# Optimization experiments

Hardware: AMD Instinct MI355X
Metric: run time of the kernel (lower is better)

Reference implementation:

```python
import jax, jax.numpy as jnp
import numpy as np

B, D = 16384, 1024
H1, H2 = 512, 256
T = 3          # num_tasks
E_SH = 2       # num_shared_experts
E_SP = 2       # num_specific_experts
G = E_SH + E_SP


def setup_inputs() -> dict:
    key = jax.random.key(0)
    ks = jax.random.split(key, 8)
    def glorot(k, shape, fan_in, fan_out):
        return jax.random.normal(k, shape, jnp.float32) * jnp.sqrt(2.0 / (fan_in + fan_out))
    return {
        "x": jax.random.normal(ks[0], (B, D), jnp.float32),
        "shared_W1": glorot(ks[1], (E_SH, D, H1), D, H1),
        "shared_b1": jnp.zeros((E_SH, H1), jnp.float32),
        "shared_W2": glorot(ks[2], (E_SH, H1, H2), H1, H2),
        "shared_b2": jnp.zeros((E_SH, H2), jnp.float32),
        "spec_W1": glorot(ks[3], (T, E_SP, D, H1), D, H1),
        "spec_b1": jnp.zeros((T, E_SP, H1), jnp.float32),
        "spec_W2": glorot(ks[4], (T, E_SP, H1, H2), H1, H2),
        "spec_b2": jnp.zeros((T, E_SP, H2), jnp.float32),
        "gate_W": glorot(ks[5], (T, D, G), D, G),
        "gate_b": jnp.zeros((T, G), jnp.float32),
    }


def reference(x, shared_W1, shared_b1, shared_W2, shared_b2,
              spec_W1, spec_b1, spec_W2, spec_b2, gate_W, gate_b):
    # Shared experts: two-layer MLP with relu, batched over experts. [B, E_SH, H2]
    sh = jax.nn.relu(jnp.einsum('bi,eih->beh', x, shared_W1) + shared_b1)
    sh = jax.nn.relu(jnp.einsum('beh,eho->beo', sh, shared_W2) + shared_b2)
    # Task-specific experts, batched over (task, expert). [B, T, E_SP, H2]
    sp = jax.nn.relu(jnp.einsum('bi,teih->bteh', x, spec_W1) + spec_b1)
    sp = jax.nn.relu(jnp.einsum('bteh,teho->bteo', sp, spec_W2) + spec_b2)
    # Gates: single linear layer per task + softmax over G=E_SH+E_SP experts. [B, T, G]
    gate = jax.nn.softmax(jnp.einsum('bi,tig->btg', x, gate_W) + gate_b, axis=-1)
    # Experts stacked in order: shared first, then specific (matches tf.stack order).
    sh_b = jnp.broadcast_to(sh[:, None], (B, T, E_SH, H2))
    experts = jnp.concatenate([sh_b, sp], axis=2)  # [B, T, G, H2]
    # Gate-weighted sum over the expert axis -> per-task outputs [B, T, H2]
    out = jnp.einsum('btgh,btg->bth', experts, gate)
    return out
```

## Files before the change

### kernel.cpp

```cpp
#include <hip/hip_runtime.h>
#include <hip/hip_bf16.h>
#include <stdint.h>

#define B_SZ 16384
#define D_SZ 1024
#define H1_SZ 512
#define H2_SZ 256
#define T_SZ 3
#define ESH 2
#define NE 8

typedef __bf16 bf16x8 __attribute__((ext_vector_type(8)));
typedef float f32x4 __attribute__((ext_vector_type(4)));
typedef unsigned short u16;
typedef u16 u16x8 __attribute__((ext_vector_type(8)));

__device__ __forceinline__ u16 f2bf(float f) {
  union { float f; uint32_t u; } v; v.f = f;
  uint32_t u = v.u;
  uint32_t r = (u + 0x7FFFu + ((u >> 16) & 1u)) >> 16;
  return (u16)r;
}
__device__ __forceinline__ float bf2f(u16 b) {
  union { uint32_t u; float f; } v; v.u = ((uint32_t)b) << 16;
  return v.f;
}

__device__ __forceinline__ void gload16(const u16* src, u16* dst_lds) {
  __builtin_amdgcn_global_load_lds(
      (const __attribute__((address_space(1))) void*)src,
      (__attribute__((address_space(3))) void*)dst_lds, 16, 0, 0);
}

__global__ __launch_bounds__(256) void cast_f32_to_bf16(
    const float* __restrict__ in, u16* __restrict__ out, int n8) {
  int i = blockIdx.x * blockDim.x + threadIdx.x;
  if (i >= n8) return;
  const float4* p = (const float4*)in + (size_t)i * 2;
  float4 a = p[0], b = p[1];
  u16x8 o;
  o[0] = f2bf(a.x); o[1] = f2bf(a.y); o[2] = f2bf(a.z); o[3] = f2bf(a.w);
  o[4] = f2bf(b.x); o[5] = f2bf(b.y); o[6] = f2bf(b.z); o[7] = f2bf(b.w);
  *((u16x8*)out + i) = o;
}

__global__ __launch_bounds__(256) void transpose_cast(
    const float* __restrict__ src, u16* __restrict__ dst, int K, int N) {
  __shared__ float tile[32][33];
  size_t e = blockIdx.z;
  const float* s = src + e * (size_t)K * N;
  u16* d = dst + e * (size_t)K * N;
  int n0 = blockIdx.x * 32, k0 = blockIdx.y * 32;
  int tx = threadIdx.x, ty = threadIdx.y;
#pragma unroll
  for (int i = ty; i < 32; i += 8)
    tile[i][tx] = s[(size_t)(k0 + i) * N + n0 + tx];
  __syncthreads();
#pragma unroll
  for (int i = ty; i < 32; i += 8)
    d[(size_t)(n0 + i) * K + k0 + tx] = f2bf(tile[tx][i]);
}

__global__ __launch_bounds__(512, 2) void gemm_ring(
    const u16* __restrict__ A, size_t strideAe,
    const u16* __restrict__ Bt,
    const float* __restrict__ bias_sh, const float* __restrict__ bias_sp,
    u16* __restrict__ C, int M, int N, int K, int ntn) {
  __shared__ __align__(16) u16 lds[4 * 16384];
  const int tid = threadIdx.x;
  const int wid = tid >> 6, lane = tid & 63;
  const int fr = lane & 15, fq = lane >> 4;
  const int wr = wid >> 2, wc = wid & 3;

  const int nwg = gridDim.x;
  const int bid = blockIdx.x;
  const int l = (bid & 7) * (nwg >> 3) + (bid >> 3);
  const int e = l & 7;
  const int rest = l >> 3;
  const int ntile = rest % ntn;
  const int mtile = rest / ntn;
  const int m0 = mtile * 256, n0 = ntile * 256;

  const u16* Ae = A + (size_t)e * strideAe;
  const u16* Be = Bt + (size_t)e * (size_t)N * K;
  const int NT = K >> 5;

  const int c0 = tid, c1 = 512 + tid;
  const int ar0 = c0 >> 2, as0 = (c0 & 3) ^ ((ar0 >> 1) & 3);
  const int ar1 = c1 >> 2, as1 = (c1 & 3) ^ ((ar1 >> 1) & 3);
  const u16* pA0 = Ae + (size_t)(m0 + ar0) * K + as0 * 8;
  const u16* pA1 = Ae + (size_t)(m0 + ar1) * K + as1 * 8;
  const u16* pB0 = Be + (size_t)(n0 + ar0) * K + as0 * 8;
  const u16* pB1 = Be + (size_t)(n0 + ar1) * K + as1 * 8;
  const int dst0 = (wid * 64) * 8;
  const int dst1 = (512 + wid * 64) * 8;

  int offA[8], offB[4];
#pragma unroll
  for (int m = 0; m < 8; ++m) {
    int r = wr * 128 + m * 16 + fr;
    offA[m] = r * 32 + ((fq ^ ((r >> 1) & 3)) * 8);
  }
#pragma unroll
  for (int n = 0; n < 4; ++n) {
    int cg = wc * 64 + n * 16 + fr;
    offB[n] = 8192 + cg * 32 + ((fq ^ ((cg >> 1) & 3)) * 8);
  }

  f32x4 acc[8][4] = {};

#define STAGE(t) do { const int sbs = ((t) & 3) * 16384;              \
    gload16(pA0 + (t) * 32, &lds[sbs + dst0]);                        \
    gload16(pA1 + (t) * 32, &lds[sbs + dst1]);                        \
    gload16(pB0 + (t) * 32, &lds[sbs + 8192 + dst0]);                 \
    gload16(pB1 + (t) * 32, &lds[sbs + 8192 + dst1]); } while (0)

  STAGE(0); STAGE(1); STAGE(2);
  asm volatile("s_waitcnt vmcnt(8)");
  __builtin_amdgcn_s_barrier();
  __builtin_amdgcn_sched_barrier(0);

  for (int t = 0; t < NT; ++t) {
    const u16* sl = &lds[(t & 3) * 16384];
    bf16x8 av[8], bv[4];
#pragma unroll
    for (int m = 0; m < 8; ++m) av[m] = *(const bf16x8*)&sl[offA[m]];
#pragma unroll
    for (int n = 0; n < 4; ++n) bv[n] = *(const bf16x8*)&sl[offB[n]];
    if (t + 3 < NT) STAGE(t + 3);
    __builtin_amdgcn_s_setprio(1);
#pragma unroll
    for (int m = 0; m < 8; ++m)
#pragma unroll
      for (int n = 0; n < 4; ++n)
        acc[m][n] = __builtin_amdgcn_mfma_f32_16x16x32_bf16(av[m], bv[n], acc[m][n], 0, 0, 0);
    __builtin_amdgcn_s_setprio(0);
    asm volatile("s_waitcnt vmcnt(8)");
    __builtin_amdgcn_s_barrier();
    __builtin_amdgcn_sched_barrier(0);
  }
#undef STAGE

  const float* bias = (e < ESH) ? (bias_sh + (size_t)e * N)
                                : (bias_sp + (size_t)(e - ESH) * N);
  u16* Ce = C + (size_t)e * (size_t)M * N;
  float bb[4];
#pragma unroll
  for (int n = 0; n < 4; ++n) bb[n] = bias[n0 + wc * 64 + n * 16 + fr];

  const int src = (tid >> 5);
  const int cc = (tid & 31) * 8;
#pragma unroll
  for (int half = 0; half < 2; ++half) {
    if (wr == half) {
#pragma unroll
      for (int m = 0; m < 8; ++m) {
#pragma unroll
        for (int n = 0; n < 4; ++n) {
          const int col = wc * 64 + n * 16 + fr;
          f32x4 a = acc[m][n];
#pragma unroll
          for (int r = 0; r < 4; ++r) {
            float v = a[r] + bb[n];
            v = v > 0.f ? v : 0.f;
            lds[(m * 16 + fq * 4 + r) * 256 + col] = f2bf(v);
          }
        }
      }
    }
    __builtin_amdgcn_s_barrier();
#pragma unroll
    for (int pass = 0; pass < 8; ++pass) {
      const int lr = pass * 16 + src;
      const int gr = m0 + half * 128 + lr;
      u16x8 vv = *(const u16x8*)&lds[lr * 256 + cc];
      *(u16x8*)&Ce[(size_t)gr * N + n0 + cc] = vv;
    }
    __builtin_amdgcn_s_barrier();
  }
}

__global__ __launch_bounds__(256) void gates_kernel(
    const float* __restrict__ x, const float* __restrict__ gW,
    const float* __restrict__ gb, float* __restrict__ gates) {
  __shared__ float gw[12][1024];
  const int tid = threadIdx.x;
  for (int i = tid; i < 12 * 1024; i += 256) {
    int tg = i >> 10, k = i & 1023;
    gw[tg][k] = gW[(size_t)(tg >> 2) * 4096 + (size_t)k * 4 + (tg & 3)];
  }
  __syncthreads();
  const int wid = tid >> 6, lane = tid & 63;
  const size_t b = (size_t)blockIdx.x * 4 + wid;
  const float* xr = x + b * 1024;
  float acc[12] = {};
  for (int kk = 0; kk < 16; ++kk) {
    float xv = xr[kk * 64 + lane];
#pragma unroll
    for (int t = 0; t < 12; ++t) acc[t] += xv * gw[t][kk * 64 + lane];
  }
#pragma unroll
  for (int off = 32; off >= 1; off >>= 1)
#pragma unroll
    for (int t = 0; t < 12; ++t) acc[t] += __shfl_xor(acc[t], off);
  if (lane == 0) {
    float* gr = gates + b * 12;
#pragma unroll
    for (int t = 0; t < 3; ++t) {
      float l0 = acc[t * 4 + 0] + gb[t * 4 + 0];
      float l1 = acc[t * 4 + 1] + gb[t * 4 + 1];
      float l2 = acc[t * 4 + 2] + gb[t * 4 + 2];
      float l3 = acc[t * 4 + 3] + gb[t * 4 + 3];
      float mx = fmaxf(fmaxf(l0, l1), fmaxf(l2, l3));
      float e0 = __expf(l0 - mx), e1 = __expf(l1 - mx);
      float e2 = __expf(l2 - mx), e3 = __expf(l3 - mx);
      float inv = 1.f / (e0 + e1 + e2 + e3);
      gr[t * 4 + 0] = e0 * inv; gr[t * 4 + 1] = e1 * inv;
      gr[t * 4 + 2] = e2 * inv; gr[t * 4 + 3] = e3 * inv;
    }
  }
}

__global__ __launch_bounds__(256) void combine_kernel(
    const u16* __restrict__ y2, const float* __restrict__ gates,
    float* __restrict__ out) {
  const int tid = threadIdx.x;
  const int rb = tid >> 5;
  const int hc = (tid & 31) * 8;
  const size_t b = (size_t)blockIdx.x * 8 + rb;
  const float* g = gates + b * 12;
  float acc0[8] = {}, acc1[8] = {}, acc2[8] = {};
#pragma unroll
  for (int e = 0; e < 8; ++e) {
    u16x8 v = *(const u16x8*)&y2[(size_t)e * B_SZ * H2_SZ + b * H2_SZ + hc];
    float f[8];
#pragma unroll
    for (int i = 0; i < 8; ++i) f[i] = bf2f(v[i]);
    if (e < 2) {
      float g0 = g[0 * 4 + e], g1 = g[1 * 4 + e], g2 = g[2 * 4 + e];
#pragma unroll
      for (int i = 0; i < 8; ++i) {
        acc0[i] += g0 * f[i]; acc1[i] += g1 * f[i]; acc2[i] += g2 * f[i];
      }
    } else {
      const int t = (e - 2) >> 1, gi = 2 + ((e - 2) & 1);
      float gv = g[t * 4 + gi];
      float* acc = (t == 0) ? acc0 : (t == 1) ? acc1 : acc2;
#pragma unroll
      for (int i = 0; i < 8; ++i) acc[i] += gv * f[i];
    }
  }
  float* o = out + b * (3 * 256);
  *(float4*)&o[0 * 256 + hc]     = make_float4(acc0[0], acc0[1], acc0[2], acc0[3]);
  *(float4*)&o[0 * 256 + hc + 4] = make_float4(acc0[4], acc0[5], acc0[6], acc0[7]);
  *(float4*)&o[1 * 256 + hc]     = make_float4(acc1[0], acc1[1], acc1[2], acc1[3]);
  *(float4*)&o[1 * 256 + hc + 4] = make_float4(acc1[4], acc1[5], acc1[6], acc1[7]);
  *(float4*)&o[2 * 256 + hc]     = make_float4(acc2[0], acc2[1], acc2[2], acc2[3]);
  *(float4*)&o[2 * 256 + hc + 4] = make_float4(acc2[4], acc2[5], acc2[6], acc2[7]);
}

extern "C" void kernel_launch(void* const* d_in, const int* in_sizes, int n_in,
                              void* d_out, int out_size, void* d_ws, size_t ws_size,
                              hipStream_t stream) {
  (void)in_sizes; (void)n_in; (void)out_size; (void)ws_size;
  const float* x   = (const float*)d_in[0];
  const float* sW1 = (const float*)d_in[1];
  const float* sb1 = (const float*)d_in[2];
  const float* sW2 = (const float*)d_in[3];
  const float* sb2 = (const float*)d_in[4];
  const float* pW1 = (const float*)d_in[5];
  const float* pb1 = (const float*)d_in[6];
  const float* pW2 = (const float*)d_in[7];
  const float* pb2 = (const float*)d_in[8];
  const float* gW  = (const float*)d_in[9];
  const float* gb  = (const float*)d_in[10];

  uint8_t* ws = (uint8_t*)d_ws;
  u16* xb    = (u16*)(ws);
  u16* w1t   = (u16*)(ws + 33554432);
  u16* w2t   = (u16*)(ws + 41943040);
  u16* y1    = (u16*)(ws + 44040192);
  u16* y2    = (u16*)(ws + 178257920);
  float* gts = (float*)(ws + 245366784);

  cast_f32_to_bf16<<<(B_SZ * D_SZ / 8 + 255) / 256, 256, 0, stream>>>(
      x, xb, B_SZ * D_SZ / 8);

  transpose_cast<<<dim3(512 / 32, 1024 / 32, 2), dim3(32, 8), 0, stream>>>(
      sW1, w1t, 1024, 512);
  transpose_cast<<<dim3(512 / 32, 1024 / 32, 6), dim3(32, 8), 0, stream>>>(
      pW1, w1t + (size_t)2 * 1024 * 512, 1024, 512);
  transpose_cast<<<dim3(256 / 32, 512 / 32, 2), dim3(32, 8), 0, stream>>>(
      sW2, w2t, 512, 256);
  transpose_cast<<<dim3(256 / 32, 512 / 32, 6), dim3(32, 8), 0, stream>>>(
      pW2, w2t + (size_t)2 * 512 * 256, 512, 256);

  gates_kernel<<<B_SZ / 4, 256, 0, stream>>>(x, gW, gb, gts);

  gemm_ring<<<(B_SZ / 256) * (512 / 256) * NE, 512, 0, stream>>>(
      xb, 0, w1t, sb1, pb1, y1, B_SZ, 512, 1024, 512 / 256);

  gemm_ring<<<(B_SZ / 256) * (256 / 256) * NE, 512, 0, stream>>>(
      y1, (size_t)B_SZ * 512, w2t, sb2, pb2, y2, B_SZ, 256, 512, 256 / 256);

  combine_kernel<<<B_SZ / 8, 256, 0, stream>>>(y2, gts, (float*)d_out);
}
```

Before: 324.1 us.

## Fuse preprocessing kernels and split GEMM K-loop into two-phase pipelined halves

Merges the four weight transpose-cast launches into one kernel and folds the x-to-bf16 cast into the gates kernel, so x is read once and fewer launches are issued. The GEMM is replaced by a two-phase variant. Each K-step splits the A loads and MFMAs into halves with interleaved barriers, and prefetch depth drops from 3 to 2 stages. The block-to-tile mapping no longer uses the XCD-aware remap, and the epilogue LDS row stride is padded to 264 to reduce bank conflicts. The extra barriers and shallower prefetch may expose memory latency, and dropping the remap may hurt L2 locality.

```diff
diff --git a/kernel.cpp b/kernel.cpp
--- a/kernel.cpp
+++ b/kernel.cpp
@@ -32,24 +32,26 @@
       (__attribute__((address_space(3))) void*)dst_lds, 16, 0, 0);
 }
 
-__global__ __launch_bounds__(256) void cast_f32_to_bf16(
-    const float* __restrict__ in, u16* __restrict__ out, int n8) {
-  int i = blockIdx.x * blockDim.x + threadIdx.x;
-  if (i >= n8) return;
-  const float4* p = (const float4*)in + (size_t)i * 2;
-  float4 a = p[0], b = p[1];
-  u16x8 o;
-  o[0] = f2bf(a.x); o[1] = f2bf(a.y); o[2] = f2bf(a.z); o[3] = f2bf(a.w);
-  o[4] = f2bf(b.x); o[5] = f2bf(b.y); o[6] = f2bf(b.z); o[7] = f2bf(b.w);
-  *((u16x8*)out + i) = o;
-}
-
-__global__ __launch_bounds__(256) void transpose_cast(
-    const float* __restrict__ src, u16* __restrict__ dst, int K, int N) {
+__global__ __launch_bounds__(256) void transpose_cast_all(
+    const float* __restrict__ sW1, const float* __restrict__ pW1,
+    const float* __restrict__ sW2, const float* __restrict__ pW2,
+    u16* __restrict__ w1t, u16* __restrict__ w2t) {
   __shared__ float tile[32][33];
-  size_t e = blockIdx.z;
-  const float* s = src + e * (size_t)K * N;
-  u16* d = dst + e * (size_t)K * N;
+  const int z = blockIdx.z;
+  int K, N;
+  const float* s;
+  u16* d;
+  if (z < 8) {
+    K = 1024; N = 512;
+    s = (z < 2) ? (sW1 + (size_t)z * K * N) : (pW1 + (size_t)(z - 2) * K * N);
+    d = w1t + (size_t)z * K * N;
+  } else {
+    K = 512; N = 256;
+    const int e = z - 8;
+    if (blockIdx.x >= 8 || blockIdx.y >= 16) return;
+    s = (e < 2) ? (sW2 + (size_t)e * K * N) : (pW2 + (size_t)(e - 2) * K * N);
+    d = w2t + (size_t)e * K * N;
+  }
   int n0 = blockIdx.x * 32, k0 = blockIdx.y * 32;
   int tx = threadIdx.x, ty = threadIdx.y;
 #pragma unroll
@@ -61,128 +63,10 @@
     d[(size_t)(n0 + i) * K + k0 + tx] = f2bf(tile[tx][i]);
 }
 
-__global__ __launch_bounds__(512, 2) void gemm_ring(
-    const u16* __restrict__ A, size_t strideAe,
-    const u16* __restrict__ Bt,
-    const float* __restrict__ bias_sh, const float* __restrict__ bias_sp,
-    u16* __restrict__ C, int M, int N, int K, int ntn) {
-  __shared__ __align__(16) u16 lds[4 * 16384];
-  const int tid = threadIdx.x;
-  const int wid = tid >> 6, lane = tid & 63;
-  const int fr = lane & 15, fq = lane >> 4;
-  const int wr = wid >> 2, wc = wid & 3;
-
-  const int nwg = gridDim.x;
-  const int bid = blockIdx.x;
-  const int l = (bid & 7) * (nwg >> 3) + (bid >> 3);
-  const int e = l & 7;
-  const int rest = l >> 3;
-  const int ntile = rest % ntn;
-  const int mtile = rest / ntn;
-  const int m0 = mtile * 256, n0 = ntile * 256;
-
-  const u16* Ae = A + (size_t)e * strideAe;
-  const u16* Be = Bt + (size_t)e * (size_t)N * K;
-  const int NT = K >> 5;
-
-  const int c0 = tid, c1 = 512 + tid;
-  const int ar0 = c0 >> 2, as0 = (c0 & 3) ^ ((ar0 >> 1) & 3);
-  const int ar1 = c1 >> 2, as1 = (c1 & 3) ^ ((ar1 >> 1) & 3);
-  const u16* pA0 = Ae + (size_t)(m0 + ar0) * K + as0 * 8;
-  const u16* pA1 = Ae + (size_t)(m0 + ar1) * K + as1 * 8;
-  const u16* pB0 = Be + (size_t)(n0 + ar0) * K + as0 * 8;
-  const u16* pB1 = Be + (size_t)(n0 + ar1) * K + as1 * 8;
-  const int dst0 = (wid * 64) * 8;
-  const int dst1 = (512 + wid * 64) * 8;
-
-  int offA[8], offB[4];
-#pragma unroll
-  for (int m = 0; m < 8; ++m) {
-    int r = wr * 128 + m * 16 + fr;
-    offA[m] = r * 32 + ((fq ^ ((r >> 1) & 3)) * 8);
-  }
-#pragma unroll
-  for (int n = 0; n < 4; ++n) {
-    int cg = wc * 64 + n * 16 + fr;
-    offB[n] = 8192 + cg * 32 + ((fq ^ ((cg >> 1) & 3)) * 8);
-  }
-
-  f32x4 acc[8][4] = {};
-
-#define STAGE(t) do { const int sbs = ((t) & 3) * 16384;              \
-    gload16(pA0 + (t) * 32, &lds[sbs + dst0]);                        \
-    gload16(pA1 + (t) * 32, &lds[sbs + dst1]);                        \
-    gload16(pB0 + (t) * 32, &lds[sbs + 8192 + dst0]);                 \
-    gload16(pB1 + (t) * 32, &lds[sbs + 8192 + dst1]); } while (0)
-
-  STAGE(0); STAGE(1); STAGE(2);
-  asm volatile("s_waitcnt vmcnt(8)");
-  __builtin_amdgcn_s_barrier();
-  __builtin_amdgcn_sched_barrier(0);
-
-  for (int t = 0; t < NT; ++t) {
-    const u16* sl = &lds[(t & 3) * 16384];
-    bf16x8 av[8], bv[4];
-#pragma unroll
-    for (int m = 0; m < 8; ++m) av[m] = *(const bf16x8*)&sl[offA[m]];
-#pragma unroll
-    for (int n = 0; n < 4; ++n) bv[n] = *(const bf16x8*)&sl[offB[n]];
-    if (t + 3 < NT) STAGE(t + 3);
-    __builtin_amdgcn_s_setprio(1);
-#pragma unroll
-    for (int m = 0; m < 8; ++m)
-#pragma unroll
-      for (int n = 0; n < 4; ++n)
-        acc[m][n] = __builtin_amdgcn_mfma_f32_16x16x32_bf16(av[m], bv[n], acc[m][n], 0, 0, 0);
-    __builtin_amdgcn_s_setprio(0);
-    asm volatile("s_waitcnt vmcnt(8)");
-    __builtin_amdgcn_s_barrier();
-    __builtin_amdgcn_sched_barrier(0);
-  }
-#undef STAGE
-
-  const float* bias = (e < ESH) ? (bias_sh + (size_t)e * N)
-                                : (bias_sp + (size_t)(e - ESH) * N);
-  u16* Ce = C + (size_t)e * (size_t)M * N;
-  float bb[4];
-#pragma unroll
-  for (int n = 0; n < 4; ++n) bb[n] = bias[n0 + wc * 64 + n * 16 + fr];
-
-  const int src = (tid >> 5);
-  const int cc = (tid & 31) * 8;
-#pragma unroll
-  for (int half = 0; half < 2; ++half) {
-    if (wr == half) {
-#pragma unroll
-      for (int m = 0; m < 8; ++m) {
-#pragma unroll
-        for (int n = 0; n < 4; ++n) {
-          const int col = wc * 64 + n * 16 + fr;
-          f32x4 a = acc[m][n];
-#pragma unroll
-          for (int r = 0; r < 4; ++r) {
-            float v = a[r] + bb[n];
-            v = v > 0.f ? v : 0.f;
-            lds[(m * 16 + fq * 4 + r) * 256 + col] = f2bf(v);
-          }
-        }
-      }
-    }
-    __builtin_amdgcn_s_barrier();
-#pragma unroll
-    for (int pass = 0; pass < 8; ++pass) {
-      const int lr = pass * 16 + src;
-      const int gr = m0 + half * 128 + lr;
-      u16x8 vv = *(const u16x8*)&lds[lr * 256 + cc];
-      *(u16x8*)&Ce[(size_t)gr * N + n0 + cc] = vv;
-    }
-    __builtin_amdgcn_s_barrier();
-  }
-}
-
-__global__ __launch_bounds__(256) void gates_kernel(
+__global__ __launch_bounds__(256) void gates_cast_kernel(
     const float* __restrict__ x, const float* __restrict__ gW,
-    const float* __restrict__ gb, float* __restrict__ gates) {
+    const float* __restrict__ gb, float* __restrict__ gates,
+    u16* __restrict__ xb) {
   __shared__ float gw[12][1024];
   const int tid = threadIdx.x;
   for (int i = tid; i < 12 * 1024; i += 256) {
@@ -193,9 +77,11 @@
   const int wid = tid >> 6, lane = tid & 63;
   const size_t b = (size_t)blockIdx.x * 4 + wid;
   const float* xr = x + b * 1024;
+  u16* xbr = xb + b * 1024;
   float acc[12] = {};
   for (int kk = 0; kk < 16; ++kk) {
     float xv = xr[kk * 64 + lane];
+    xbr[kk * 64 + lane] = f2bf(xv);
 #pragma unroll
     for (int t = 0; t < 12; ++t) acc[t] += xv * gw[t][kk * 64 + lane];
   }
@@ -218,6 +104,145 @@
       gr[t * 4 + 0] = e0 * inv; gr[t * 4 + 1] = e1 * inv;
       gr[t * 4 + 2] = e2 * inv; gr[t * 4 + 3] = e3 * inv;
     }
+  }
+}
+
+__global__ __launch_bounds__(512, 2) void gemm_2ph(
+    const u16* __restrict__ A, size_t strideAe,
+    const u16* __restrict__ Bt,
+    const float* __restrict__ bias_sh, const float* __restrict__ bias_sp,
+    u16* __restrict__ C, int M, int N, int K, int ntn_sh) {
+  __shared__ __align__(16) u16 lds[4 * 16384];
+  const int tid = threadIdx.x;
+  const int wid = tid >> 6, lane = tid & 63;
+  const int fr = lane & 15, fq = lane >> 4;
+  const int wr = wid >> 2, wc = wid & 3;
+
+  const int bid = blockIdx.x;
+  const int e = bid & 7;
+  const int rest = bid >> 3;
+  const int mtile = rest >> ntn_sh;
+  const int ntile = rest & ((1 << ntn_sh) - 1);
+  const int m0 = mtile * 256, n0 = ntile * 256;
+
+  const u16* Ae = A + (size_t)e * strideAe;
+  const u16* Be = Bt + (size_t)e * (size_t)N * K;
+  const int NT = K >> 5;
+
+  const int srow = tid >> 2;
+  const int sslot = (tid & 3) ^ ((tid >> 3) & 3);
+  const u16* pA[2];
+  const u16* pB[2];
+#pragma unroll
+  for (int h = 0; h < 2; ++h) {
+    pA[h] = Ae + (size_t)(m0 + h * 128 + srow) * K + sslot * 8;
+    pB[h] = Be + (size_t)(n0 + h * 128 + srow) * K + sslot * 8;
+  }
+  const int wdst = wid * 512;
+
+  int offA[8], offB[4];
+#pragma unroll
+  for (int m = 0; m < 8; ++m) {
+    int rr = wr * 128 + m * 16 + fr;
+    offA[m] = rr * 32 + ((fq ^ ((fr >> 1) & 3)) * 8);
+  }
+#pragma unroll
+  for (int n = 0; n < 4; ++n) {
+    int cg = wc * 64 + n * 16 + fr;
+    offB[n] = 8192 + cg * 32 + ((fq ^ ((fr >> 1) & 3)) * 8);
+  }
+
+  f32x4 acc[8][4] = {};
+
+#define STG_A(t) do { const int sbs = ((t) & 3) * 16384;                    \
+    gload16(pA[0] + (size_t)(t) * 32, &lds[sbs + wdst]);                    \
+    gload16(pA[1] + (size_t)(t) * 32, &lds[sbs + 4096 + wdst]); } while (0)
+#define STG_B(t) do { const int sbs = ((t) & 3) * 16384 + 8192;             \
+    gload16(pB[0] + (size_t)(t) * 32, &lds[sbs + wdst]);                    \
+    gload16(pB[1] + (size_t)(t) * 32, &lds[sbs + 4096 + wdst]); } while (0)
+
+  STG_A(0); STG_B(0);
+  STG_A(1); STG_B(1);
+  asm volatile("s_waitcnt vmcnt(4)");
+  __builtin_amdgcn_s_barrier();
+  __builtin_amdgcn_sched_barrier(0);
+
+  for (int t = 0; t < NT; ++t) {
+    const u16* sl = &lds[(t & 3) * 16384];
+    bf16x8 av[4], bv[4];
+#pragma unroll
+    for (int m = 0; m < 4; ++m) av[m] = *(const bf16x8*)&sl[offA[m]];
+#pragma unroll
+    for (int n = 0; n < 4; ++n) bv[n] = *(const bf16x8*)&sl[offB[n]];
+    if (t + 2 < NT) STG_A(t + 2);
+    __builtin_amdgcn_s_barrier();
+    asm volatile("s_waitcnt lgkmcnt(0)");
+    __builtin_amdgcn_sched_barrier(0);
+    __builtin_amdgcn_s_setprio(1);
+#pragma unroll
+    for (int m = 0; m < 4; ++m)
+#pragma unroll
+      for (int n = 0; n < 4; ++n)
+        acc[m][n] = __builtin_amdgcn_mfma_f32_16x16x32_bf16(av[m], bv[n], acc[m][n], 0, 0, 0);
+    __builtin_amdgcn_s_setprio(0);
+    __builtin_amdgcn_s_barrier();
+    bf16x8 aw[4];
+#pragma unroll
+    for (int m = 0; m < 4; ++m) aw[m] = *(const bf16x8*)&sl[offA[4 + m]];
+    if (t + 2 < NT) STG_B(t + 2);
+    if (t + 2 < NT)      asm volatile("s_waitcnt vmcnt(4)");
+    else if (t + 1 < NT) asm volatile("s_waitcnt vmcnt(0)");
+    __builtin_amdgcn_s_barrier();
+    asm volatile("s_waitcnt lgkmcnt(0)");
+    __builtin_amdgcn_sched_barrier(0);
+    __builtin_amdgcn_s_setprio(1);
+#pragma unroll
+    for (int m = 0; m < 4; ++m)
+#pragma unroll
+      for (int n = 0; n < 4; ++n)
+        acc[4 + m][n] = __builtin_amdgcn_mfma_f32_16x16x32_bf16(aw[m], bv[n], acc[4 + m][n], 0, 0, 0);
+    __builtin_amdgcn_s_setprio(0);
+    __builtin_amdgcn_s_barrier();
+  }
+#undef STG_A
+#undef STG_B
+
+  const float* bias = (e < ESH) ? (bias_sh + (size_t)e * N)
+                                : (bias_sp + (size_t)(e - ESH) * N);
+  u16* Ce = C + (size_t)e * (size_t)M * N;
+  float bb[4];
+#pragma unroll
+  for (int n = 0; n < 4; ++n) bb[n] = bias[n0 + wc * 64 + n * 16 + fr];
+
+  const int src = (tid >> 5);
+  const int cc = (tid & 31) * 8;
+#pragma unroll
+  for (int half = 0; half < 2; ++half) {
+    if (wr == half) {
+#pragma unroll
+      for (int m = 0; m < 8; ++m) {
+#pragma unroll
+        for (int n = 0; n < 4; ++n) {
+          const int col = wc * 64 + n * 16 + fr;
+          f32x4 a = acc[m][n];
+#pragma unroll
+          for (int rr = 0; rr < 4; ++rr) {
+            float v = a[rr] + bb[n];
+            v = v > 0.f ? v : 0.f;
+            lds[(m * 16 + fq * 4 + rr) * 264 + col] = f2bf(v);
+          }
+        }
+      }
+    }
+    __builtin_amdgcn_s_barrier();
+#pragma unroll
+    for (int pass = 0; pass < 8; ++pass) {
+      const int lr = pass * 16 + src;
+      const int gr = m0 + half * 128 + lr;
+      u16x8 vv = *(const u16x8*)&lds[lr * 264 + cc];
+      *(u16x8*)&Ce[(size_t)gr * N + n0 + cc] = vv;
+    }
+    __builtin_amdgcn_s_barrier();
   }
 }
 
@@ -283,25 +308,16 @@
   u16* y2    = (u16*)(ws + 178257920);
   float* gts = (float*)(ws + 245366784);
 
-  cast_f32_to_bf16<<<(B_SZ * D_SZ / 8 + 255) / 256, 256, 0, stream>>>(
-      x, xb, B_SZ * D_SZ / 8);
-
-  transpose_cast<<<dim3(512 / 32, 1024 / 32, 2), dim3(32, 8), 0, stream>>>(
-      sW1, w1t, 1024, 512);
-  transpose_cast<<<dim3(512 / 32, 1024 / 32, 6), dim3(32, 8), 0, stream>>>(
-      pW1, w1t + (size_t)2 * 1024 * 512, 1024, 512);
-  transpose_cast<<<dim3(256 / 32, 512 / 32, 2), dim3(32, 8), 0, stream>>>(
-      sW2, w2t, 512, 256);
-  transpose_cast<<<dim3(256 / 32, 512 / 32, 6), dim3(32, 8), 0, stream>>>(
-      pW2, w2t + (size_t)2 * 512 * 256, 512, 256);
-
-  gates_kernel<<<B_SZ / 4, 256, 0, stream>>>(x, gW, gb, gts);
-
-  gemm_ring<<<(B_SZ / 256) * (512 / 256) * NE, 512, 0, stream>>>(
-      xb, 0, w1t, sb1, pb1, y1, B_SZ, 512, 1024, 512 / 256);
-
-  gemm_ring<<<(B_SZ / 256) * (256 / 256) * NE, 512, 0, stream>>>(
-      y1, (size_t)B_SZ * 512, w2t, sb2, pb2, y2, B_SZ, 256, 512, 256 / 256);
+  transpose_cast_all<<<dim3(16, 32, 16), dim3(32, 8), 0, stream>>>(
+      sW1, pW1, sW2, pW2, w1t, w2t);
+
+  gates_cast_kernel<<<B_SZ / 4, 256, 0, stream>>>(x, gW, gb, gts, xb);
+
+  gemm_2ph<<<(B_SZ / 256) * (512 / 256) * NE, 512, 0, stream>>>(
+      xb, 0, w1t, sb1, pb1, y1, B_SZ, 512, 1024, 1);
+
+  gemm_2ph<<<(B_SZ / 256) * (256 / 256) * NE, 512, 0, stream>>>(
+      y1, (size_t)B_SZ * 512, w2t, sb2, pb2, y2, B_SZ, 256, 512, 0);
 
   combine_kernel<<<B_SZ / 8, 256, 0, stream>>>(y2, gts, (float*)d_out);
 }
```

Result: faster. 297.0 us (-8.4%).
